# Kernel optimization log

Measured on AMD Instinct MI355X. Metric: run time of the kernel, lower is better.

The kernel has to match this reference:

```python
import jax, jax.numpy as jnp
import numpy as np
import string

N_QUBITS = 16
N_LAYERS = 2
BATCH = 32
DIM = 2 ** N_QUBITS


def _apply_1q(psi, U, q):
    # psi: (B,) + (2,)*n complex; U: (2,2) complex acting on qubit q
    n = psi.ndim - 1
    ax = string.ascii_lowercase[:n]
    out = list(ax)
    out[q] = 'A'
    return jnp.einsum('A' + ax[q] + ',z' + ax + '->z' + ''.join(out), U, psi)


def _apply_2q(psi, G, c, t):
    # G: (2,2,2,2) = (out_c, out_t, in_c, in_t)
    n = psi.ndim - 1
    ax = string.ascii_lowercase[:n]
    out = list(ax)
    out[c] = 'A'
    out[t] = 'B'
    return jnp.einsum('AB' + ax[c] + ax[t] + ',z' + ax + '->z' + ''.join(out), G, psi)


def _rx(th):
    c = jnp.cos(th * 0.5).astype(jnp.complex64)
    s = jnp.sin(th * 0.5).astype(jnp.complex64)
    return jnp.array([[c, -1j * s], [-1j * s, c]])


def _ry(th):
    c = jnp.cos(th * 0.5).astype(jnp.complex64)
    s = jnp.sin(th * 0.5).astype(jnp.complex64)
    return jnp.array([[c, -s], [s, c]])


def _rz(th):
    th_c = th.astype(jnp.complex64)
    z = jnp.zeros((), jnp.complex64)
    return jnp.array([[jnp.exp(-0.5j * th_c), z], [z, jnp.exp(0.5j * th_c)]])


_CNOT = jnp.array([[1, 0, 0, 0],
                   [0, 1, 0, 0],
                   [0, 0, 0, 1],
                   [0, 0, 1, 0]], dtype=jnp.complex64).reshape(2, 2, 2, 2)


def setup_inputs() -> dict:
    key = jax.random.key(0)
    k1, k2, k3 = jax.random.split(key, 3)
    thetas = jax.random.normal(k1, (N_LAYERS, 3, N_QUBITS), dtype=jnp.float32)
    re = jax.random.normal(k2, (BATCH, DIM), dtype=jnp.float32)
    im = jax.random.normal(k3, (BATCH, DIM), dtype=jnp.float32)
    norm = jnp.sqrt(jnp.sum(re * re + im * im, axis=-1, keepdims=True))
    return {"thetas": thetas, "state_re": re / norm, "state_im": im / norm}


def reference(thetas, state_re, state_im):
    B = state_re.shape[0]
    psi = (state_re.astype(jnp.complex64) + 1j * state_im.astype(jnp.complex64))
    psi = psi.reshape((B,) + (2,) * N_QUBITS)
    for l in range(N_LAYERS):
        for q in range(N_QUBITS):
            psi = _apply_1q(psi, _rx(thetas[l, 0, q]), q)
            psi = _apply_1q(psi, _ry(thetas[l, 1, q]), q)
            psi = _apply_1q(psi, _rz(thetas[l, 2, q]), q)
        for q in range(N_QUBITS):
            psi = _apply_2q(psi, _CNOT, q, (q + 1) % N_QUBITS)
    probs = (psi.real ** 2 + psi.imag ** 2).reshape(B, -1)
    return probs
```

## Files before the change

### kernel.cpp

```cpp
#include <hip/hip_runtime.h>


#define NT 256

__device__ __forceinline__ int fperm(int x) {
  int y = x ^ (x >> 1);
  y ^= (x & 1) ? 0xC000 : 0;
  return y & 0xFFFF;
}

__device__ __forceinline__ int finv16(int x) {
  int s = x;
  s ^= s >> 1; s ^= s >> 2; s ^= s >> 4; s ^= s >> 8;
  int b15 = ((s ^ (s >> 15)) & 1) << 15;
  return (s & 0x7FFF) | b15;
}

__device__ __forceinline__ int swz1(int l) { return l ^ ((l >> 4) & 31); }
__device__ __forceinline__ int swz2(int l) { return l ^ ((l >> 5) & 31); }

__device__ __forceinline__ void compute_gates(const float* __restrict__ th, float* gsh) {
  int tid = threadIdx.x;
  if (tid < 32) {
    int l = tid >> 4, q = tid & 15;
    float tx = th[l * 48 + q], ty = th[l * 48 + 16 + q], tz = th[l * 48 + 32 + q];
    float cx, sx, cy, sy, cz, sz;
    sincosf(0.5f * tx, &sx, &cx);
    sincosf(0.5f * ty, &sy, &cy);
    sincosf(0.5f * tz, &sz, &cz);
    float m00r = cy * cx, m00i =  sy * sx;
    float m01r = -sy * cx, m01i = -cy * sx;
    float m10r =  sy * cx, m10i = -cy * sx;
    float m11r =  cy * cx, m11i = -sy * sx;
    float* G = gsh + tid * 8;
    G[0] = cz * m00r + sz * m00i;  G[1] = cz * m00i - sz * m00r;
    G[2] = cz * m01r + sz * m01i;  G[3] = cz * m01i - sz * m01r;
    G[4] = cz * m10r - sz * m10i;  G[5] = cz * m10i + sz * m10r;
    G[6] = cz * m11r - sz * m11i;  G[7] = cz * m11i + sz * m11r;
  }
}

template <int MK, int SK, int N>
__device__ __forceinline__ void greg(float (&ar)[N], float (&ai)[N],
                                     const float* G, int c) {
  const float4* G4 = (const float4*)G;
  float4 r0 = G4[0], r1 = G4[1];
  bool sw = (c != 0);
  float h00r = sw ? r1.z : r0.x, h00i = sw ? r1.w : r0.y;
  float h01r = sw ? r1.x : r0.z, h01i = sw ? r1.y : r0.w;
  float h10r = sw ? r0.z : r1.x, h10i = sw ? r0.w : r1.y;
  float h11r = sw ? r0.x : r1.z, h11i = sw ? r0.y : r1.w;
  constexpr int PV = MK & (-MK);
#pragma unroll
  for (int k = 0; k < N; k++) {
    if (k & PV) continue;
    const int k2 = k ^ MK;
    const int p0 = __builtin_popcount(k & SK) & 1;
    const int ka = p0 ? k2 : k;
    const int kb = p0 ? k : k2;
    float xr = ar[ka], xi = ai[ka], yr = ar[kb], yi = ai[kb];
    ar[ka] = h00r * xr - h00i * xi + h01r * yr - h01i * yi;
    ai[ka] = h00r * xi + h00i * xr + h01r * yi + h01i * yr;
    ar[kb] = h10r * xr - h10i * xi + h11r * yr - h11i * yi;
    ai[kb] = h10r * xi + h10i * xr + h11r * yi + h11i * yr;
  }
}


__device__ __forceinline__ void phaseA_body(int t, int bbase, int wb,
                                            const float* gsh,
                                            float* sre, float* sim,
                                            const float* __restrict__ xre,
                                            const float* __restrict__ xim,
                                            float2* __restrict__ ws) {
  float ar[16], ai[16];
  int base = bbase + (wb << 12);
  const float4* xr4 = (const float4*)(xre + base + (t << 4));
  const float4* xi4 = (const float4*)(xim + base + (t << 4));
#pragma unroll
  for (int q = 0; q < 4; q++) {
    float4 v = xr4[q]; ar[4*q] = v.x; ar[4*q+1] = v.y; ar[4*q+2] = v.z; ar[4*q+3] = v.w;
    float4 w = xi4[q]; ai[4*q] = w.x; ai[4*q+1] = w.y; ai[4*q+2] = w.z; ai[4*q+3] = w.w;
  }
  __syncthreads();
  greg<1, 1>(ar, ai, gsh + 15 * 8, 0);
  greg<2, 2>(ar, ai, gsh + 14 * 8, 0);
  greg<4, 4>(ar, ai, gsh + 13 * 8, 0);
  greg<8, 8>(ar, ai, gsh + 12 * 8, 0);
#pragma unroll
  for (int k = 0; k < 16; k++) { int s = swz1((t << 4) | k); sre[s] = ar[k]; sim[s] = ai[k]; }
  __syncthreads();
#pragma unroll
  for (int k = 0; k < 16; k++) {
    int s = swz1((t & 15) | (k << 4) | ((t >> 4) << 8));
    ar[k] = sre[s]; ai[k] = sim[s];
  }
  greg<1, 1>(ar, ai, gsh + 11 * 8, 0);
  greg<2, 2>(ar, ai, gsh + 10 * 8, 0);
  greg<4, 4>(ar, ai, gsh + 9 * 8, 0);
  greg<8, 8>(ar, ai, gsh + 8 * 8, 0);
#pragma unroll
  for (int k = 0; k < 16; k++) {
    int s = swz1((t & 15) | (k << 4) | ((t >> 4) << 8));
    sre[s] = ar[k]; sim[s] = ai[k];
  }
  __syncthreads();
#pragma unroll
  for (int k = 0; k < 16; k++) {
    int s = swz1(t | (k << 8)); ar[k] = sre[s]; ai[k] = sim[s];
  }
  greg<1, 1>(ar, ai, gsh + 7 * 8, 0);
  greg<2, 2>(ar, ai, gsh + 6 * 8, 0);
  greg<4, 4>(ar, ai, gsh + 5 * 8, 0);
  greg<8, 8>(ar, ai, gsh + 4 * 8, 0);
#pragma unroll
  for (int k = 0; k < 16; k++)
    ws[base + t + (k << 8)] = make_float2(ar[k], ai[k]);
}

__device__ __forceinline__ void phaseB_body(int t, int bbase, int wb,
                                            const float* gsh,
                                            float* sre, float* sim,
                                            float2* __restrict__ ws) {
  float ar[16], ai[16];
#pragma unroll
  for (int k = 0; k < 16; k++) {
    float2 v = ws[bbase + t + (wb << 8) + (k << 12)];
    ar[k] = v.x; ai[k] = v.y;
  }
  int cA = (__popc(t) + __popc(wb)) & 1;
  greg<1, 1>(ar, ai, gsh + 3 * 8, 0);
  greg<2, 2>(ar, ai, gsh + 2 * 8, 0);
  greg<4, 4>(ar, ai, gsh + 1 * 8, 0);
  greg<8, 8>(ar, ai, gsh + 0 * 8, 0);
  greg<12, 7>(ar, ai, gsh + (16 + 0) * 8, cA);
  greg<6, 12>(ar, ai, gsh + (16 + 1) * 8, 0);
  greg<3, 14>(ar, ai, gsh + (16 + 2) * 8, 0);
  __syncthreads();
#pragma unroll
  for (int k = 0; k < 16; k++) {
    int s = swz2(t | (k << 8)); sre[s] = ar[k]; sim[s] = ai[k];
  }
  __syncthreads();
#pragma unroll
  for (int k = 0; k < 16; k++) {
    int s = swz2((k & 3) | (t << 2) | ((k >> 2) << 10));
    ar[k] = sre[s]; ai[k] = sim[s];
  }
  greg<13, 15>(ar, ai, gsh + (16 + 15) * 8, cA);
  greg<3, 14>(ar, ai, gsh + (16 + 14) * 8, cA);
#pragma unroll
  for (int k = 0; k < 16; k++) {
    int s = swz2((k & 3) | (t << 2) | ((k >> 2) << 10));
    sre[s] = ar[k]; sim[s] = ai[k];
  }
  __syncthreads();
#pragma unroll
  for (int k = 0; k < 16; k++) {
    int s = swz2((t & 1) | (k << 1) | ((t >> 1) << 5));
    ar[k] = sre[s]; ai[k] = sim[s];
  }
  {
    int cC = (__popc(t >> 1) + __popc(wb)) & 1;
    greg<3, 14>(ar, ai, gsh + (16 + 13) * 8, cC);
    greg<6, 12>(ar, ai, gsh + (16 + 12) * 8, cC);
    greg<12, 8>(ar, ai, gsh + (16 + 11) * 8, cC);
  }
#pragma unroll
  for (int k = 0; k < 16; k++) {
    int s = swz2((t & 1) | (k << 1) | ((t >> 1) << 5));
    sre[s] = ar[k]; sim[s] = ai[k];
  }
  __syncthreads();
#pragma unroll
  for (int k = 0; k < 16; k++) {
    int s = swz2((t & 15) | (k << 4) | ((t >> 4) << 8));
    ar[k] = sre[s]; ai[k] = sim[s];
  }
  {
    int cD = (__popc(t >> 4) + __popc(wb)) & 1;
    greg<3, 14>(ar, ai, gsh + (16 + 10) * 8, cD);
    greg<6, 12>(ar, ai, gsh + (16 + 9) * 8, cD);
    greg<12, 8>(ar, ai, gsh + (16 + 8) * 8, cD);
  }
#pragma unroll
  for (int k = 0; k < 16; k++) {
    int full = (t & 15) | (k << 4) | (wb << 8) | ((t >> 4) << 12);
    ws[bbase + full] = make_float2(ar[k], ai[k]);
  }
}

__device__ __forceinline__ void phaseC_body(int t, int bbase3, int g3,
                                            const float* gsh,
                                            const float2* __restrict__ ws,
                                            float* __restrict__ out) {
  int jt = t | (g3 << 13);
  float br[32], bi[32];
#pragma unroll
  for (int k = 0; k < 32; k++) {
    int j = jt | (k << 8);
    float2 v = ws[bbase3 + fperm(j)];
    br[k] = v.x; bi[k] = v.y;
  }
  greg<1, 1>(br, bi, gsh + (16 + 7) * 8, 0);
  greg<2, 2>(br, bi, gsh + (16 + 6) * 8, 0);
  greg<4, 4>(br, bi, gsh + (16 + 5) * 8, 0);
  greg<8, 8>(br, bi, gsh + (16 + 4) * 8, 0);
  greg<16, 16>(br, bi, gsh + (16 + 3) * 8, 0);
#pragma unroll
  for (int k = 0; k < 32; k++) {
    int j = jt | (k << 8);
    out[bbase3 + finv16(j)] = br[k] * br[k] + bi[k] * bi[k];
  }
}


__global__ void __launch_bounds__(NT) pass1_k(const float* __restrict__ th,
                                              const float* __restrict__ xre,
                                              const float* __restrict__ xim,
                                              float2* __restrict__ ws) {
  __shared__ float gsh[256];
  __shared__ float sre[4096], sim[4096];
  int t = threadIdx.x;
  int blk = blockIdx.x, batch = blk >> 4, wb = blk & 15;
  compute_gates(th, gsh);
  phaseA_body(t, batch * 65536, wb, gsh, sre, sim, xre, xim, ws);
}

__global__ void __launch_bounds__(NT) pass2_k(const float* __restrict__ th,
                                              float2* __restrict__ ws) {
  __shared__ float gsh[256];
  __shared__ float sre[4096], sim[4096];
  int t = threadIdx.x;
  int blk = blockIdx.x, batch = blk >> 4, wb = blk & 15;
  compute_gates(th, gsh);
  __syncthreads();
  phaseB_body(t, batch * 65536, wb, gsh, sre, sim, ws);
}

__global__ void __launch_bounds__(NT) pass3_k(const float* __restrict__ th,
                                              const float2* __restrict__ ws,
                                              float* __restrict__ out) {
  __shared__ float gsh[256];
  int t = threadIdx.x;
  int blk = blockIdx.x, batch = blk >> 3, g3 = blk & 7;
  compute_gates(th, gsh);
  __syncthreads();
  phaseC_body(t, batch * 65536, g3, gsh, ws, out);
}


__device__ __forceinline__ void signal(unsigned* cnt) {
  __threadfence();
  __syncthreads();
  if (threadIdx.x == 0)
    __hip_atomic_fetch_add(cnt, 1u, __ATOMIC_RELEASE, __HIP_MEMORY_SCOPE_AGENT);
}

__device__ __forceinline__ void wait16(unsigned* cnt) {
  if (threadIdx.x == 0) {
    while (__hip_atomic_load(cnt, __ATOMIC_ACQUIRE, __HIP_MEMORY_SCOPE_AGENT) < 16u)
      __builtin_amdgcn_s_sleep(1);
  }
  __syncthreads();
  __threadfence();
}

__global__ void __launch_bounds__(NT, 2)
fused_k(const float* __restrict__ th,
        const float* __restrict__ xre, const float* __restrict__ xim,
        float2* __restrict__ ws, float* __restrict__ out,
        unsigned* __restrict__ cnt1, unsigned* __restrict__ cnt2) {
  __shared__ float gsh[256];
  __shared__ float sre[4096], sim[4096];
  int t = threadIdx.x;
  int blk = blockIdx.x;
  int batch = blk >> 4, wb = blk & 15;
  int bbase = batch * 65536;

  compute_gates(th, gsh);
  phaseA_body(t, bbase, wb, gsh, sre, sim, xre, xim, ws);
  signal(&cnt1[batch]);

  wait16(&cnt1[batch]);
  phaseB_body(t, bbase, wb, gsh, sre, sim, ws);
  signal(&cnt2[batch]);

  if (blk >= 256) return;
  int batch3 = blk >> 3, g3 = blk & 7;
  wait16(&cnt2[batch3]);
  phaseC_body(t, batch3 * 65536, g3, gsh, ws, out);
}


extern "C" void kernel_launch(void* const* d_in, const int* in_sizes, int n_in,
                              void* d_out, int out_size, void* d_ws, size_t ws_size,
                              hipStream_t stream) {
  const float* th  = (const float*)d_in[0];
  const float* xre = (const float*)d_in[1];
  const float* xim = (const float*)d_in[2];
  float* out = (float*)d_out;

  float2* amp = (float2*)d_ws;
  unsigned* cnt1 = (unsigned*)((char*)d_ws + (16u << 20));
  unsigned* cnt2 = cnt1 + 32;

  int maxBlk = 0;
  hipError_t qrc = hipOccupancyMaxActiveBlocksPerMultiprocessor(
      &maxBlk, (const void*)fused_k, NT, 0);
  bool try_coop = (qrc == hipSuccess && maxBlk >= 2);

  bool coop_ok = false;
  if (try_coop) {
    hipMemsetAsync((void*)cnt1, 0, 64 * sizeof(unsigned), stream);
    void* args[] = {(void*)&th, (void*)&xre, (void*)&xim,
                    (void*)&amp, (void*)&out, (void*)&cnt1, (void*)&cnt2};
    hipError_t rc = hipLaunchCooperativeKernel((const void*)fused_k, dim3(512),
                                               dim3(NT), args, 0, stream);
    coop_ok = (rc == hipSuccess);
  }

  if (!coop_ok) {
    pass1_k<<<512, NT, 0, stream>>>(th, xre, xim, amp);
    pass2_k<<<512, NT, 0, stream>>>(th, amp);
    pass3_k<<<256, NT, 0, stream>>>(th, amp, out);
  }
}
```

Baseline: 104.0 us.

## Interleave complex LDS storage, spread phase C over all blocks, pad counters

Amplitudes now live as interleaved float2 in registers and LDS, with a new 16-entry XOR swizzle, instead of split real/imag arrays. Phase C is redone so all 512 blocks take part, each with 16 amplitudes and an extra LDS transpose, rather than half the blocks holding 32 registers each. Blocks are remapped so consecutive block IDs span different batches. The per-batch sync counters are padded to separate cache lines, and the spin-wait sleep is longer. The aim is fewer LDS instructions, better balance and register pressure in the last phase, and less counter contention, at the cost of an extra barrier and possible bank conflicts from the new swizzle.

```diff
diff --git a/kernel.cpp b/kernel.cpp
--- a/kernel.cpp
+++ b/kernel.cpp
@@ -16,8 +16,7 @@
   return (s & 0x7FFF) | b15;
 }
 
-__device__ __forceinline__ int swz1(int l) { return l ^ ((l >> 4) & 31); }
-__device__ __forceinline__ int swz2(int l) { return l ^ ((l >> 5) & 31); }
+__device__ __forceinline__ int swz(int l) { return l ^ ((l >> 4) & 15); }
 
 __device__ __forceinline__ void compute_gates(const float* __restrict__ th, float* gsh) {
   int tid = threadIdx.x;
@@ -41,8 +40,7 @@
 }
 
 template <int MK, int SK, int N>
-__device__ __forceinline__ void greg(float (&ar)[N], float (&ai)[N],
-                                     const float* G, int c) {
+__device__ __forceinline__ void greg(float2 (&a)[N], const float* G, int c) {
   const float4* G4 = (const float4*)G;
   float4 r0 = G4[0], r1 = G4[1];
   bool sw = (c != 0);
@@ -58,195 +56,182 @@
     const int p0 = __builtin_popcount(k & SK) & 1;
     const int ka = p0 ? k2 : k;
     const int kb = p0 ? k : k2;
-    float xr = ar[ka], xi = ai[ka], yr = ar[kb], yi = ai[kb];
-    ar[ka] = h00r * xr - h00i * xi + h01r * yr - h01i * yi;
-    ai[ka] = h00r * xi + h00i * xr + h01r * yi + h01i * yr;
-    ar[kb] = h10r * xr - h10i * xi + h11r * yr - h11i * yi;
-    ai[kb] = h10r * xi + h10i * xr + h11r * yi + h11i * yr;
+    float2 x = a[ka], y = a[kb];
+    a[ka] = make_float2(h00r * x.x - h00i * x.y + h01r * y.x - h01i * y.y,
+                        h00r * x.y + h00i * x.x + h01r * y.y + h01i * y.x);
+    a[kb] = make_float2(h10r * x.x - h10i * x.y + h11r * y.x - h11i * y.y,
+                        h10r * x.y + h10i * x.x + h11r * y.y + h11i * y.x);
   }
 }
 
 
 __device__ __forceinline__ void phaseA_body(int t, int bbase, int wb,
-                                            const float* gsh,
-                                            float* sre, float* sim,
+                                            const float* gsh, float2* samp,
                                             const float* __restrict__ xre,
                                             const float* __restrict__ xim,
                                             float2* __restrict__ ws) {
-  float ar[16], ai[16];
+  float2 a[16];
   int base = bbase + (wb << 12);
   const float4* xr4 = (const float4*)(xre + base + (t << 4));
   const float4* xi4 = (const float4*)(xim + base + (t << 4));
 #pragma unroll
   for (int q = 0; q < 4; q++) {
-    float4 v = xr4[q]; ar[4*q] = v.x; ar[4*q+1] = v.y; ar[4*q+2] = v.z; ar[4*q+3] = v.w;
-    float4 w = xi4[q]; ai[4*q] = w.x; ai[4*q+1] = w.y; ai[4*q+2] = w.z; ai[4*q+3] = w.w;
-  }
-  __syncthreads();
-  greg<1, 1>(ar, ai, gsh + 15 * 8, 0);
-  greg<2, 2>(ar, ai, gsh + 14 * 8, 0);
-  greg<4, 4>(ar, ai, gsh + 13 * 8, 0);
-  greg<8, 8>(ar, ai, gsh + 12 * 8, 0);
-#pragma unroll
-  for (int k = 0; k < 16; k++) { int s = swz1((t << 4) | k); sre[s] = ar[k]; sim[s] = ai[k]; }
-  __syncthreads();
-#pragma unroll
-  for (int k = 0; k < 16; k++) {
-    int s = swz1((t & 15) | (k << 4) | ((t >> 4) << 8));
-    ar[k] = sre[s]; ai[k] = sim[s];
-  }
-  greg<1, 1>(ar, ai, gsh + 11 * 8, 0);
-  greg<2, 2>(ar, ai, gsh + 10 * 8, 0);
-  greg<4, 4>(ar, ai, gsh + 9 * 8, 0);
-  greg<8, 8>(ar, ai, gsh + 8 * 8, 0);
-#pragma unroll
-  for (int k = 0; k < 16; k++) {
-    int s = swz1((t & 15) | (k << 4) | ((t >> 4) << 8));
-    sre[s] = ar[k]; sim[s] = ai[k];
-  }
-  __syncthreads();
-#pragma unroll
-  for (int k = 0; k < 16; k++) {
-    int s = swz1(t | (k << 8)); ar[k] = sre[s]; ai[k] = sim[s];
-  }
-  greg<1, 1>(ar, ai, gsh + 7 * 8, 0);
-  greg<2, 2>(ar, ai, gsh + 6 * 8, 0);
-  greg<4, 4>(ar, ai, gsh + 5 * 8, 0);
-  greg<8, 8>(ar, ai, gsh + 4 * 8, 0);
-#pragma unroll
-  for (int k = 0; k < 16; k++)
-    ws[base + t + (k << 8)] = make_float2(ar[k], ai[k]);
+    float4 v = xr4[q], w = xi4[q];
+    a[4*q+0] = make_float2(v.x, w.x); a[4*q+1] = make_float2(v.y, w.y);
+    a[4*q+2] = make_float2(v.z, w.z); a[4*q+3] = make_float2(v.w, w.w);
+  }
+  __syncthreads();
+  greg<1, 1>(a, gsh + 15 * 8, 0);
+  greg<2, 2>(a, gsh + 14 * 8, 0);
+  greg<4, 4>(a, gsh + 13 * 8, 0);
+  greg<8, 8>(a, gsh + 12 * 8, 0);
+#pragma unroll
+  for (int k = 0; k < 16; k++) samp[swz((t << 4) | k)] = a[k];
+  __syncthreads();
+#pragma unroll
+  for (int k = 0; k < 16; k++)
+    a[k] = samp[swz((t & 15) | (k << 4) | ((t >> 4) << 8))];
+  greg<1, 1>(a, gsh + 11 * 8, 0);
+  greg<2, 2>(a, gsh + 10 * 8, 0);
+  greg<4, 4>(a, gsh + 9 * 8, 0);
+  greg<8, 8>(a, gsh + 8 * 8, 0);
+#pragma unroll
+  for (int k = 0; k < 16; k++)
+    samp[swz((t & 15) | (k << 4) | ((t >> 4) << 8))] = a[k];
+  __syncthreads();
+#pragma unroll
+  for (int k = 0; k < 16; k++) a[k] = samp[swz(t | (k << 8))];
+  greg<1, 1>(a, gsh + 7 * 8, 0);
+  greg<2, 2>(a, gsh + 6 * 8, 0);
+  greg<4, 4>(a, gsh + 5 * 8, 0);
+  greg<8, 8>(a, gsh + 4 * 8, 0);
+#pragma unroll
+  for (int k = 0; k < 16; k++)
+    ws[base + t + (k << 8)] = a[k];
 }
 
 __device__ __forceinline__ void phaseB_body(int t, int bbase, int wb,
-                                            const float* gsh,
-                                            float* sre, float* sim,
+                                            const float* gsh, float2* samp,
                                             float2* __restrict__ ws) {
-  float ar[16], ai[16];
-#pragma unroll
-  for (int k = 0; k < 16; k++) {
-    float2 v = ws[bbase + t + (wb << 8) + (k << 12)];
-    ar[k] = v.x; ai[k] = v.y;
-  }
+  float2 a[16];
+#pragma unroll
+  for (int k = 0; k < 16; k++)
+    a[k] = ws[bbase + t + (wb << 8) + (k << 12)];
   int cA = (__popc(t) + __popc(wb)) & 1;
-  greg<1, 1>(ar, ai, gsh + 3 * 8, 0);
-  greg<2, 2>(ar, ai, gsh + 2 * 8, 0);
-  greg<4, 4>(ar, ai, gsh + 1 * 8, 0);
-  greg<8, 8>(ar, ai, gsh + 0 * 8, 0);
-  greg<12, 7>(ar, ai, gsh + (16 + 0) * 8, cA);
-  greg<6, 12>(ar, ai, gsh + (16 + 1) * 8, 0);
-  greg<3, 14>(ar, ai, gsh + (16 + 2) * 8, 0);
-  __syncthreads();
-#pragma unroll
-  for (int k = 0; k < 16; k++) {
-    int s = swz2(t | (k << 8)); sre[s] = ar[k]; sim[s] = ai[k];
-  }
-  __syncthreads();
-#pragma unroll
-  for (int k = 0; k < 16; k++) {
-    int s = swz2((k & 3) | (t << 2) | ((k >> 2) << 10));
-    ar[k] = sre[s]; ai[k] = sim[s];
-  }
-  greg<13, 15>(ar, ai, gsh + (16 + 15) * 8, cA);
-  greg<3, 14>(ar, ai, gsh + (16 + 14) * 8, cA);
-#pragma unroll
-  for (int k = 0; k < 16; k++) {
-    int s = swz2((k & 3) | (t << 2) | ((k >> 2) << 10));
-    sre[s] = ar[k]; sim[s] = ai[k];
-  }
-  __syncthreads();
-#pragma unroll
-  for (int k = 0; k < 16; k++) {
-    int s = swz2((t & 1) | (k << 1) | ((t >> 1) << 5));
-    ar[k] = sre[s]; ai[k] = sim[s];
-  }
+  greg<1, 1>(a, gsh + 3 * 8, 0);
+  greg<2, 2>(a, gsh + 2 * 8, 0);
+  greg<4, 4>(a, gsh + 1 * 8, 0);
+  greg<8, 8>(a, gsh + 0 * 8, 0);
+  greg<12, 7>(a, gsh + (16 + 0) * 8, cA);
+  greg<6, 12>(a, gsh + (16 + 1) * 8, 0);
+  greg<3, 14>(a, gsh + (16 + 2) * 8, 0);
+  __syncthreads();
+#pragma unroll
+  for (int k = 0; k < 16; k++) samp[swz(t | (k << 8))] = a[k];
+  __syncthreads();
+#pragma unroll
+  for (int k = 0; k < 16; k++)
+    a[k] = samp[swz((k & 3) | (t << 2) | ((k >> 2) << 10))];
+  greg<13, 15>(a, gsh + (16 + 15) * 8, cA);
+  greg<3, 14>(a, gsh + (16 + 14) * 8, cA);
+#pragma unroll
+  for (int k = 0; k < 16; k++)
+    samp[swz((k & 3) | (t << 2) | ((k >> 2) << 10))] = a[k];
+  __syncthreads();
+#pragma unroll
+  for (int k = 0; k < 16; k++)
+    a[k] = samp[swz((t & 1) | (k << 1) | ((t >> 1) << 5))];
   {
     int cC = (__popc(t >> 1) + __popc(wb)) & 1;
-    greg<3, 14>(ar, ai, gsh + (16 + 13) * 8, cC);
-    greg<6, 12>(ar, ai, gsh + (16 + 12) * 8, cC);
-    greg<12, 8>(ar, ai, gsh + (16 + 11) * 8, cC);
-  }
-#pragma unroll
-  for (int k = 0; k < 16; k++) {
-    int s = swz2((t & 1) | (k << 1) | ((t >> 1) << 5));
-    sre[s] = ar[k]; sim[s] = ai[k];
-  }
-  __syncthreads();
-#pragma unroll
-  for (int k = 0; k < 16; k++) {
-    int s = swz2((t & 15) | (k << 4) | ((t >> 4) << 8));
-    ar[k] = sre[s]; ai[k] = sim[s];
-  }
+    greg<3, 14>(a, gsh + (16 + 13) * 8, cC);
+    greg<6, 12>(a, gsh + (16 + 12) * 8, cC);
+    greg<12, 8>(a, gsh + (16 + 11) * 8, cC);
+  }
+#pragma unroll
+  for (int k = 0; k < 16; k++)
+    samp[swz((t & 1) | (k << 1) | ((t >> 1) << 5))] = a[k];
+  __syncthreads();
+#pragma unroll
+  for (int k = 0; k < 16; k++)
+    a[k] = samp[swz((t & 15) | (k << 4) | ((t >> 4) << 8))];
   {
     int cD = (__popc(t >> 4) + __popc(wb)) & 1;
-    greg<3, 14>(ar, ai, gsh + (16 + 10) * 8, cD);
-    greg<6, 12>(ar, ai, gsh + (16 + 9) * 8, cD);
-    greg<12, 8>(ar, ai, gsh + (16 + 8) * 8, cD);
+    greg<3, 14>(a, gsh + (16 + 10) * 8, cD);
+    greg<6, 12>(a, gsh + (16 + 9) * 8, cD);
+    greg<12, 8>(a, gsh + (16 + 8) * 8, cD);
   }
 #pragma unroll
   for (int k = 0; k < 16; k++) {
     int full = (t & 15) | (k << 4) | (wb << 8) | ((t >> 4) << 12);
-    ws[bbase + full] = make_float2(ar[k], ai[k]);
-  }
-}
-
-__device__ __forceinline__ void phaseC_body(int t, int bbase3, int g3,
-                                            const float* gsh,
+    ws[bbase + full] = a[k];
+  }
+}
+
+__device__ __forceinline__ void phaseC_body(int t, int bbase, int wb,
+                                            const float* gsh, float2* samp,
                                             const float2* __restrict__ ws,
                                             float* __restrict__ out) {
-  int jt = t | (g3 << 13);
-  float br[32], bi[32];
-#pragma unroll
-  for (int k = 0; k < 32; k++) {
-    int j = jt | (k << 8);
-    float2 v = ws[bbase3 + fperm(j)];
-    br[k] = v.x; bi[k] = v.y;
-  }
-  greg<1, 1>(br, bi, gsh + (16 + 7) * 8, 0);
-  greg<2, 2>(br, bi, gsh + (16 + 6) * 8, 0);
-  greg<4, 4>(br, bi, gsh + (16 + 5) * 8, 0);
-  greg<8, 8>(br, bi, gsh + (16 + 4) * 8, 0);
-  greg<16, 16>(br, bi, gsh + (16 + 3) * 8, 0);
-#pragma unroll
-  for (int k = 0; k < 32; k++) {
-    int j = jt | (k << 8);
-    out[bbase3 + finv16(j)] = br[k] * br[k] + bi[k] * bi[k];
-  }
-}
-
-
-__global__ void __launch_bounds__(NT) pass1_k(const float* __restrict__ th,
-                                              const float* __restrict__ xre,
-                                              const float* __restrict__ xim,
-                                              float2* __restrict__ ws) {
+  int fix = ((wb & 1) << 7) | ((wb >> 1) << 13);
+  int jt = (t & 127) | ((t >> 7) << 8) | fix;
+  float2 a[16];
+#pragma unroll
+  for (int k = 0; k < 16; k++) {
+    int j = jt | (k << 9);
+    a[k] = ws[bbase + fperm(j)];
+  }
+  greg<1, 1>(a, gsh + (16 + 6) * 8, 0);
+  greg<2, 2>(a, gsh + (16 + 5) * 8, 0);
+  greg<4, 4>(a, gsh + (16 + 4) * 8, 0);
+  greg<8, 8>(a, gsh + (16 + 3) * 8, 0);
+#pragma unroll
+  for (int k = 0; k < 16; k++) samp[swz(t | (k << 8))] = a[k];
+  __syncthreads();
+#pragma unroll
+  for (int k = 0; k < 16; k++)
+    a[k] = samp[swz((t & 127) | (k << 7) | ((t >> 7) << 11))];
+  greg<1, 1>(a, gsh + (16 + 7) * 8, 0);
+#pragma unroll
+  for (int k = 0; k < 16; k++) {
+    int l = (t & 127) | (k << 7) | ((t >> 7) << 11);
+    int j = (l & 127) | (((l >> 7) & 1) << 8) | ((l >> 8) << 9) | fix;
+    out[bbase + finv16(j)] = a[k].x * a[k].x + a[k].y * a[k].y;
+  }
+}
+
+
+__global__ void __launch_bounds__(NT, 2) pass1_k(const float* __restrict__ th,
+                                                 const float* __restrict__ xre,
+                                                 const float* __restrict__ xim,
+                                                 float2* __restrict__ ws) {
   __shared__ float gsh[256];
-  __shared__ float sre[4096], sim[4096];
-  int t = threadIdx.x;
-  int blk = blockIdx.x, batch = blk >> 4, wb = blk & 15;
+  __shared__ float2 samp[4096];
+  int t = threadIdx.x, blk = blockIdx.x;
+  int batch = (blk & 7) + ((blk >> 7) << 3), wb = (blk >> 3) & 15;
   compute_gates(th, gsh);
-  phaseA_body(t, batch * 65536, wb, gsh, sre, sim, xre, xim, ws);
-}
-
-__global__ void __launch_bounds__(NT) pass2_k(const float* __restrict__ th,
-                                              float2* __restrict__ ws) {
+  phaseA_body(t, batch << 16, wb, gsh, samp, xre, xim, ws);
+}
+
+__global__ void __launch_bounds__(NT, 2) pass2_k(const float* __restrict__ th,
+                                                 float2* __restrict__ ws) {
   __shared__ float gsh[256];
-  __shared__ float sre[4096], sim[4096];
-  int t = threadIdx.x;
-  int blk = blockIdx.x, batch = blk >> 4, wb = blk & 15;
+  __shared__ float2 samp[4096];
+  int t = threadIdx.x, blk = blockIdx.x;
+  int batch = (blk & 7) + ((blk >> 7) << 3), wb = (blk >> 3) & 15;
   compute_gates(th, gsh);
   __syncthreads();
-  phaseB_body(t, batch * 65536, wb, gsh, sre, sim, ws);
-}
-
-__global__ void __launch_bounds__(NT) pass3_k(const float* __restrict__ th,
-                                              const float2* __restrict__ ws,
-                                              float* __restrict__ out) {
+  phaseB_body(t, batch << 16, wb, gsh, samp, ws);
+}
+
+__global__ void __launch_bounds__(NT, 2) pass3_k(const float* __restrict__ th,
+                                                 const float2* __restrict__ ws,
+                                                 float* __restrict__ out) {
   __shared__ float gsh[256];
-  int t = threadIdx.x;
-  int blk = blockIdx.x, batch = blk >> 3, g3 = blk & 7;
+  __shared__ float2 samp[4096];
+  int t = threadIdx.x, blk = blockIdx.x;
+  int batch = (blk & 7) + ((blk >> 7) << 3), wb = (blk >> 3) & 15;
   compute_gates(th, gsh);
   __syncthreads();
-  phaseC_body(t, batch * 65536, g3, gsh, ws, out);
+  phaseC_body(t, batch << 16, wb, gsh, samp, ws, out);
 }
 
 
@@ -260,7 +245,7 @@
 __device__ __forceinline__ void wait16(unsigned* cnt) {
   if (threadIdx.x == 0) {
     while (__hip_atomic_load(cnt, __ATOMIC_ACQUIRE, __HIP_MEMORY_SCOPE_AGENT) < 16u)
-      __builtin_amdgcn_s_sleep(1);
+      __builtin_amdgcn_s_sleep(2);
   }
   __syncthreads();
   __threadfence();
@@ -272,24 +257,21 @@
         float2* __restrict__ ws, float* __restrict__ out,
         unsigned* __restrict__ cnt1, unsigned* __restrict__ cnt2) {
   __shared__ float gsh[256];
-  __shared__ float sre[4096], sim[4096];
-  int t = threadIdx.x;
-  int blk = blockIdx.x;
-  int batch = blk >> 4, wb = blk & 15;
-  int bbase = batch * 65536;
+  __shared__ float2 samp[4096];
+  int t = threadIdx.x, blk = blockIdx.x;
+  int batch = (blk & 7) + ((blk >> 7) << 3), wb = (blk >> 3) & 15;
+  int bbase = batch << 16;
 
   compute_gates(th, gsh);
-  phaseA_body(t, bbase, wb, gsh, sre, sim, xre, xim, ws);
-  signal(&cnt1[batch]);
-
-  wait16(&cnt1[batch]);
-  phaseB_body(t, bbase, wb, gsh, sre, sim, ws);
-  signal(&cnt2[batch]);
-
-  if (blk >= 256) return;
-  int batch3 = blk >> 3, g3 = blk & 7;
-  wait16(&cnt2[batch3]);
-  phaseC_body(t, batch3 * 65536, g3, gsh, ws, out);
+  phaseA_body(t, bbase, wb, gsh, samp, xre, xim, ws);
+  signal(&cnt1[batch << 5]);
+
+  wait16(&cnt1[batch << 5]);
+  phaseB_body(t, bbase, wb, gsh, samp, ws);
+  signal(&cnt2[batch << 5]);
+
+  wait16(&cnt2[batch << 5]);
+  phaseC_body(t, bbase, wb, gsh, samp, ws, out);
 }
 
 
@@ -303,7 +285,7 @@
 
   float2* amp = (float2*)d_ws;
   unsigned* cnt1 = (unsigned*)((char*)d_ws + (16u << 20));
-  unsigned* cnt2 = cnt1 + 32;
+  unsigned* cnt2 = cnt1 + 1024;
 
   int maxBlk = 0;
   hipError_t qrc = hipOccupancyMaxActiveBlocksPerMultiprocessor(
@@ -312,7 +294,7 @@
 
   bool coop_ok = false;
   if (try_coop) {
-    hipMemsetAsync((void*)cnt1, 0, 64 * sizeof(unsigned), stream);
+    hipMemsetAsync((void*)cnt1, 0, 2048 * sizeof(unsigned), stream);
     void* args[] = {(void*)&th, (void*)&xre, (void*)&xim,
                     (void*)&amp, (void*)&out, (void*)&cnt1, (void*)&cnt2};
     hipError_t rc = hipLaunchCooperativeKernel((const void*)fused_k, dim3(512),
@@ -323,6 +305,6 @@
   if (!coop_ok) {
     pass1_k<<<512, NT, 0, stream>>>(th, xre, xim, amp);
     pass2_k<<<512, NT, 0, stream>>>(th, amp);
-    pass3_k<<<256, NT, 0, stream>>>(th, amp, out);
-  }
-}
+    pass3_k<<<512, NT, 0, stream>>>(th, amp, out);
+  }
+}
```

Result: slower. 106.8 us (+2.6%).
